# Kernel optimization log

Hardware: AMD Instinct MI355X
Metric: run time of the kernel (lower is better)

Reference implementation:

```python
import jax, jax.numpy as jnp
import numpy as np

ALPHA = 1.0
BLOCK = 128  # row block size for the pairwise L1 reduction


def _pairwise_score(features, a):
    # score[i, j] = sum_k |f[i,k] - f[j,k]| * a[k]
    # computed in row blocks to avoid the O(n^2*d) broadcast intermediate
    n, d = features.shape
    av = a[:, 0]  # [d]
    fb = features.reshape(n // BLOCK, BLOCK, d)

    def blk(fblk):  # fblk: [B, d]
        diff = jnp.abs(fblk[:, None, :] - features[None, :, :])  # [B, n, d]
        return jnp.einsum('bnd,d->bn', diff, av)                  # [B, n]

    return jax.lax.map(blk, fb).reshape(n, n)


def setup_inputs() -> dict:
    key = jax.random.key(0)
    n, d = 8192, 256
    features = jax.random.normal(key, (n, d), dtype=jnp.float32)
    a = jnp.full((d, 1), 0.01, dtype=jnp.float32)  # nn.init.constant_(a, 0.01)
    return {"features": features, "a": a}


def reference(features, a):
    score = _pairwise_score(features, a)                 # [n, n]
    adjacency = jnp.exp(-ALPHA * jax.nn.relu(score))     # [n, n]
    # D^{-1/2} A D^{-1/2} via row/col elementwise scaling (== diag mm mm)
    dsq = jnp.sum(adjacency, axis=1) ** -0.5             # [n]
    normalized = dsq[:, None] * adjacency * dsq[None, :]
    return (normalized, adjacency)
```

## Files before the change

kernel.cpp:

```cpp
#include <hip/hip_runtime.h>
#include <math.h>

typedef unsigned int uint;
typedef float f32x4 __attribute__((ext_vector_type(4)));

__device__ __forceinline__ uint fenc(float f) {
    uint u = __float_as_uint(f);
    return (u & 0x80000000u) ? ~u : (u | 0x80000000u);
}
__device__ __forceinline__ float fdec(uint u) {
    uint v = (u & 0x80000000u) ? (u & 0x7FFFFFFFu) : ~u;
    return __uint_as_float(v);
}

__device__ __forceinline__ void ntst(float* p, float a, float b, float c, float d) {
    f32x4 t; t.x = a; t.y = b; t.z = c; t.w = d;
    __builtin_nontemporal_store(t, (f32x4*)p);
}

__global__ __launch_bounds__(256) void init_kernel(uint* __restrict__ flags,
                                                   const float* __restrict__ A,
                                                   int d)
{
    const int t = threadIdx.x;
    if (t == 0) { flags[0] = 0u; flags[1] = 0xFFFFFFFFu; flags[2] = 0u; }
    __syncthreads();
    for (int k = t; k < d; k += 256)
        if (A[k] < 0.f) atomicOr(&flags[0], 1u);
}

__global__ __launch_bounds__(256) void minmax_kernel(const float* __restrict__ F,
                                                     const float* __restrict__ A,
                                                     uint* __restrict__ flags,
                                                     int n, int d)
{
    const int total4 = n * d / 4;
    float lmin = 3.4e38f, lmax = -3.4e38f;
    for (int e4 = blockIdx.x * 256 + threadIdx.x; e4 < total4; e4 += gridDim.x * 256) {
        int e = e4 * 4;
        int dk = e % d;
        float4 f = *(const float4*)(F + e);
        float4 a = *(const float4*)(A + dk);
        float g0 = fabsf(a.x) * f.x, g1 = fabsf(a.y) * f.y;
        float g2 = fabsf(a.z) * f.z, g3 = fabsf(a.w) * f.w;
        lmin = fminf(lmin, fminf(fminf(g0, g1), fminf(g2, g3)));
        lmax = fmaxf(lmax, fmaxf(fmaxf(g0, g1), fmaxf(g2, g3)));
    }
    #pragma unroll
    for (int m = 1; m < 64; m <<= 1) {
        lmin = fminf(lmin, __shfl_xor(lmin, m));
        lmax = fmaxf(lmax, __shfl_xor(lmax, m));
    }
    if ((threadIdx.x & 63) == 0) {
        atomicMin(&flags[1], fenc(lmin));
        atomicMax(&flags[2], fenc(lmax));
    }
}

__global__ __launch_bounds__(256) void quant_kernel(const float* __restrict__ F,
                                                    const float* __restrict__ A,
                                                    const uint* __restrict__ flags,
                                                    uint* __restrict__ Q,
                                                    float* __restrict__ rowsum,
                                                    int n, int d)
{
    const int t = threadIdx.x;
    const int r = blockIdx.x * 32 + (t & 31);
    if (t < 32) rowsum[blockIdx.x * 32 + t] = 0.f;
    const int kqb = t >> 5;
    const int d4 = d >> 2;
    const float gmin = fdec(flags[1]), gmax = fdec(flags[2]);
    const float span = gmax - gmin;
    const float inv = span > 0.f ? 255.f / span : 0.f;
    for (int kq = kqb; kq < d4; kq += 8) {
        float4 f = *(const float4*)(F + (size_t)r * d + kq * 4);
        float4 a = *(const float4*)(A + kq * 4);
        uint q0 = 0, q1 = 0, q2 = 0, q3 = 0;
        if (a.x > 0.f) q0 = (uint)fminf(fmaxf((a.x * f.x - gmin) * inv + 0.5f, 0.f), 255.f);
        if (a.y > 0.f) q1 = (uint)fminf(fmaxf((a.y * f.y - gmin) * inv + 0.5f, 0.f), 255.f);
        if (a.z > 0.f) q2 = (uint)fminf(fmaxf((a.z * f.z - gmin) * inv + 0.5f, 0.f), 255.f);
        if (a.w > 0.f) q3 = (uint)fminf(fmaxf((a.w * f.w - gmin) * inv + 0.5f, 0.f), 255.f);
        Q[(size_t)kq * n + r] = q0 | (q1 << 8) | (q2 << 16) | (q3 << 24);
    }
}

__device__ __forceinline__ void sad_core(const uint* __restrict__ Q, int n, int chunks,
                                         int i0, int j0, int t,
                                         uint (&acc)[8][8],
                                         uint (&As)[16][128], uint (&Bs)[16][128])
{
    const int tx = t & 15, ty = t >> 4;
    const int kk0 = t >> 5;
    const int col = 4 * (t & 31);

    uint4 sa[2], sb[2];
    #pragma unroll
    for (int j = 0; j < 2; ++j) {
        size_t g = ((size_t)(kk0 + 8 * j)) * n;
        sa[j] = *(const uint4*)(Q + g + i0 + col);
        sb[j] = *(const uint4*)(Q + g + j0 + col);
    }

    for (int c = 0; c < chunks; ++c) {
        ((uint4*)&As[0][0])[t]       = sa[0];
        ((uint4*)&As[0][0])[256 + t] = sa[1];
        ((uint4*)&Bs[0][0])[t]       = sb[0];
        ((uint4*)&Bs[0][0])[256 + t] = sb[1];
        __syncthreads();

        if (c + 1 < chunks) {
            #pragma unroll
            for (int j = 0; j < 2; ++j) {
                size_t g = ((size_t)((c + 1) * 16 + kk0 + 8 * j)) * n;
                sa[j] = *(const uint4*)(Q + g + i0 + col);
                sb[j] = *(const uint4*)(Q + g + j0 + col);
            }
        }

        #pragma unroll
        for (int kk = 0; kk < 16; ++kk) {
            uint ar[8], br[8];
            *(uint4*)&ar[0] = *(const uint4*)&As[kk][4 * ty];
            *(uint4*)&ar[4] = *(const uint4*)&As[kk][64 + 4 * ty];
            *(uint4*)&br[0] = *(const uint4*)&Bs[kk][4 * tx];
            *(uint4*)&br[4] = *(const uint4*)&Bs[kk][64 + 4 * tx];
            #pragma unroll
            for (int m = 0; m < 8; ++m)
                #pragma unroll
                for (int cc = 0; cc < 8; ++cc)
                    acc[m][cc] = __builtin_amdgcn_sad_u8(ar[m], br[cc], acc[m][cc]);
        }
        __syncthreads();
    }
}

__device__ __forceinline__ void tri_decode(int b, int& bx, int& by) {
    bx = (int)((sqrtf(8.f * (float)b + 1.f) - 1.f) * 0.5f);
    while ((bx + 1) * (bx + 2) / 2 <= b) ++bx;
    while (bx * (bx + 1) / 2 > b) --bx;
    by = b - bx * (bx + 1) / 2;
}

__global__ __launch_bounds__(256, 3) void pass1_sad(const uint* __restrict__ Q,
                                                    const uint* __restrict__ flags,
                                                    float* __restrict__ adj,
                                                    float* __restrict__ rowsum,
                                                    int n, int d)
{
    if (flags[0] != 0u) return;

    __shared__ uint As[16][128];
    __shared__ uint Bs[16][128];

    int bx, by; tri_decode(blockIdx.x, bx, by);
    const int t = threadIdx.x, tx = t & 15, ty = t >> 4;
    const int i0 = by * 128, j0 = bx * 128;
    const bool diag = (bx == by);

    const float gmin = fdec(flags[1]), gmax = fdec(flags[2]);
    const float nstep = (gmin - gmax) * (1.f / 255.f);

    uint acc[8][8] = {};
    sad_core(Q, n, (d >> 2) >> 4, i0, j0, t, acc, As, Bs);

    #pragma unroll
    for (int m = 0; m < 8; ++m)
        #pragma unroll
        for (int cc = 0; cc < 8; ++cc)
            acc[m][cc] = __float_as_uint(__expf(nstep * (float)acc[m][cc]));

    #pragma unroll
    for (int m = 0; m < 8; ++m) {
        const int row = i0 + (m >> 2) * 64 + 4 * ty + (m & 3);
        #pragma unroll
        for (int qh = 0; qh < 2; ++qh)
            ntst(adj + (size_t)row * n + j0 + qh * 64 + 4 * tx,
                 __uint_as_float(acc[m][qh * 4 + 0]),
                 __uint_as_float(acc[m][qh * 4 + 1]),
                 __uint_as_float(acc[m][qh * 4 + 2]),
                 __uint_as_float(acc[m][qh * 4 + 3]));
    }

    if (!diag) {
        #pragma unroll
        for (int h = 0; h < 2; ++h)
            #pragma unroll
            for (int qh = 0; qh < 2; ++qh)
                #pragma unroll
                for (int cc = 0; cc < 4; ++cc) {
                    const int r = j0 + qh * 64 + 4 * tx + cc;
                    ntst(adj + (size_t)r * n + i0 + 64 * h + 4 * ty,
                         __uint_as_float(acc[4 * h + 0][qh * 4 + cc]),
                         __uint_as_float(acc[4 * h + 1][qh * 4 + cc]),
                         __uint_as_float(acc[4 * h + 2][qh * 4 + cc]),
                         __uint_as_float(acc[4 * h + 3][qh * 4 + cc]));
                }
    }

    #pragma unroll
    for (int m = 0; m < 8; ++m) {
        const int row = i0 + (m >> 2) * 64 + 4 * ty + (m & 3);
        float rs = 0.f;
        #pragma unroll
        for (int cc = 0; cc < 8; ++cc) rs += __uint_as_float(acc[m][cc]);
        rs += __shfl_xor(rs, 1);
        rs += __shfl_xor(rs, 2);
        rs += __shfl_xor(rs, 4);
        rs += __shfl_xor(rs, 8);
        if (tx == 0) atomicAdd(rowsum + row, rs);
    }

    if (!diag) {
        float cs[8];
        #pragma unroll
        for (int cc = 0; cc < 8; ++cc) {
            float s = 0.f;
            #pragma unroll
            for (int m = 0; m < 8; ++m) s += __uint_as_float(acc[m][cc]);
            s += __shfl_xor(s, 16);
            s += __shfl_xor(s, 32);
            cs[cc] = s;
        }
        if ((t & 48) == 0) {
            #pragma unroll
            for (int qh = 0; qh < 2; ++qh)
                #pragma unroll
                for (int cc = 0; cc < 4; ++cc)
                    atomicAdd(rowsum + j0 + qh * 64 + 4 * tx + cc, cs[qh * 4 + cc]);
        }
    }
}

__global__ __launch_bounds__(256) void adj_fp32_kernel(
    const float* __restrict__ F, const float* __restrict__ A,
    const uint* __restrict__ flags,
    float* __restrict__ adj, float* __restrict__ rowsum, int n, int d)
{
    if (flags[0] == 0u) return;

    __shared__ __align__(16) float As[32][132];
    __shared__ __align__(16) float Bs[32][132];
    __shared__ float aw[256];

    const int t  = threadIdx.x;
    const int tx = t & 15;
    const int ty = t >> 4;
    const int nb = n / 128;

    for (int k = t; k < d; k += 256) aw[k] = A[k];

    for (int bt = blockIdx.x; bt < nb * nb; bt += gridDim.x) {
        const int i0 = (bt / nb) * 128;
        const int j0 = (bt % nb) * 128;

        float acc[2][2][4][4] = {};
        const int lr = t >> 3;
        const int lk = (t & 7) << 2;

        for (int kc = 0; kc < d; kc += 32) {
            __syncthreads();
            #pragma unroll
            for (int s = 0; s < 4; ++s) {
                int r = lr + 32 * s;
                float4 v = *(const float4*)(F + (size_t)(i0 + r) * d + kc + lk);
                As[lk + 0][r] = v.x; As[lk + 1][r] = v.y;
                As[lk + 2][r] = v.z; As[lk + 3][r] = v.w;
                float4 u = *(const float4*)(F + (size_t)(j0 + r) * d + kc + lk);
                Bs[lk + 0][r] = u.x; Bs[lk + 1][r] = u.y;
                Bs[lk + 2][r] = u.z; Bs[lk + 3][r] = u.w;
            }
            __syncthreads();

            #pragma unroll
            for (int k = 0; k < 32; ++k) {
                float av[2][4], bv[2][4];
                *(float4*)&av[0][0] = *(const float4*)&As[k][4 * ty];
                *(float4*)&av[1][0] = *(const float4*)&As[k][64 + 4 * ty];
                *(float4*)&bv[0][0] = *(const float4*)&Bs[k][4 * tx];
                *(float4*)&bv[1][0] = *(const float4*)&Bs[k][64 + 4 * tx];
                const float w = aw[kc + k];
                #pragma unroll
                for (int p = 0; p < 2; ++p)
                    #pragma unroll
                    for (int m = 0; m < 4; ++m)
                        #pragma unroll
                        for (int q = 0; q < 2; ++q)
                            #pragma unroll
                            for (int c = 0; c < 4; ++c)
                                acc[p][q][m][c] += fabsf(av[p][m] - bv[q][c]) * w;
            }
        }

        #pragma unroll
        for (int p = 0; p < 2; ++p) {
            #pragma unroll
            for (int m = 0; m < 4; ++m) {
                const int row = i0 + p * 64 + ty * 4 + m;
                float rs = 0.f;
                #pragma unroll
                for (int q = 0; q < 2; ++q) {
                    float4 v;
                    v.x = __expf(-fmaxf(acc[p][q][m][0], 0.f));
                    v.y = __expf(-fmaxf(acc[p][q][m][1], 0.f));
                    v.z = __expf(-fmaxf(acc[p][q][m][2], 0.f));
                    v.w = __expf(-fmaxf(acc[p][q][m][3], 0.f));
                    rs += (v.x + v.y) + (v.z + v.w);
                    *(float4*)(adj + (size_t)row * n + j0 + q * 64 + tx * 4) = v;
                }
                rs += __shfl_xor(rs, 1);
                rs += __shfl_xor(rs, 2);
                rs += __shfl_xor(rs, 4);
                rs += __shfl_xor(rs, 8);
                if (tx == 0) atomicAdd(rowsum + row, rs);
            }
        }
        __syncthreads();
    }
}

__global__ __launch_bounds__(256) void dsq_kernel(
    const float* __restrict__ rowsum, float* __restrict__ dsq, int n)
{
    int i = blockIdx.x * 256 + threadIdx.x;
    if (i < n) dsq[i] = 1.f / sqrtf(rowsum[i]);
}

__global__ __launch_bounds__(256) void norm_kernel(
    const float* __restrict__ adj, const float* __restrict__ dsq,
    float* __restrict__ out, int n)
{
    const int i = blockIdx.y;
    const float di = dsq[i];
    const int j0 = blockIdx.x * 4096 + threadIdx.x * 4;
    #pragma unroll
    for (int k = 0; k < 4; ++k) {
        const int j = j0 + k * 1024;
        if (j >= n) return;
        f32x4 a = __builtin_nontemporal_load((const f32x4*)(adj + (size_t)i * n + j));
        float4 dj = *(const float4*)(dsq + j);
        ntst(out + (size_t)i * n + j,
             di * a.x * dj.x, di * a.y * dj.y, di * a.z * dj.z, di * a.w * dj.w);
    }
}

extern "C" void kernel_launch(void* const* d_in, const int* in_sizes, int n_in,
                              void* d_out, int out_size, void* d_ws, size_t ws_size,
                              hipStream_t stream)
{
    const float* F = (const float*)d_in[0];
    const float* A = (const float*)d_in[1];
    const int d = in_sizes[1];
    const int n = in_sizes[0] / d;

    float* nrm    = (float*)d_out;
    float* adj    = nrm + (size_t)n * n;
    uint*  flags  = (uint*)d_ws;
    float* rowsum = (float*)d_ws + 8;
    float* dsq    = rowsum + n;
    uint* Q = (uint*)d_out;

    init_kernel<<<dim3(1), dim3(256), 0, stream>>>(flags, A, d);
    minmax_kernel<<<dim3(256), dim3(256), 0, stream>>>(F, A, flags, n, d);
    quant_kernel<<<dim3(n / 32), dim3(256), 0, stream>>>(F, A, flags, Q, rowsum, n, d);

    const int nb = n / 128;
    const int tri = nb * (nb + 1) / 2;
    pass1_sad<<<dim3(tri), dim3(256), 0, stream>>>(Q, flags, adj, rowsum, n, d);
    adj_fp32_kernel<<<dim3(1024), dim3(256), 0, stream>>>(F, A, flags, adj, rowsum, n, d);

    dsq_kernel<<<dim3((n + 255) / 256), dim3(256), 0, stream>>>(rowsum, dsq, n);

    dim3 gridN((n + 4095) / 4096, n);
    norm_kernel<<<gridN, dim3(256), 0, stream>>>(adj, dsq, nrm, n);
}
```

Baseline: 299.5 us.

## Double-buffer SAD tiles, stage transposed stores via LDS, fuse dsq into norm

The SAD main loop now uses double-buffered shared memory, so the next chunk is written while the current one is consumed, with one barrier per chunk instead of two. The mirrored (transposed) adjacency writes for off-diagonal tiles are staged through a padded LDS buffer so that each row's global stores are contiguous rather than strided. The dsq kernel is removed and norm_kernel computes rsqrt of the row sums inline. The adj_fp32 grid is cut from 1024 to 304 blocks. Doubling shared memory may lower occupancy, and rsqrt is recomputed for every element.

```diff
diff --git a/kernel.cpp b/kernel.cpp
--- a/kernel.cpp
+++ b/kernel.cpp
@@ -84,56 +84,6 @@
     }
 }
 
-__device__ __forceinline__ void sad_core(const uint* __restrict__ Q, int n, int chunks,
-                                         int i0, int j0, int t,
-                                         uint (&acc)[8][8],
-                                         uint (&As)[16][128], uint (&Bs)[16][128])
-{
-    const int tx = t & 15, ty = t >> 4;
-    const int kk0 = t >> 5;
-    const int col = 4 * (t & 31);
-
-    uint4 sa[2], sb[2];
-    #pragma unroll
-    for (int j = 0; j < 2; ++j) {
-        size_t g = ((size_t)(kk0 + 8 * j)) * n;
-        sa[j] = *(const uint4*)(Q + g + i0 + col);
-        sb[j] = *(const uint4*)(Q + g + j0 + col);
-    }
-
-    for (int c = 0; c < chunks; ++c) {
-        ((uint4*)&As[0][0])[t]       = sa[0];
-        ((uint4*)&As[0][0])[256 + t] = sa[1];
-        ((uint4*)&Bs[0][0])[t]       = sb[0];
-        ((uint4*)&Bs[0][0])[256 + t] = sb[1];
-        __syncthreads();
-
-        if (c + 1 < chunks) {
-            #pragma unroll
-            for (int j = 0; j < 2; ++j) {
-                size_t g = ((size_t)((c + 1) * 16 + kk0 + 8 * j)) * n;
-                sa[j] = *(const uint4*)(Q + g + i0 + col);
-                sb[j] = *(const uint4*)(Q + g + j0 + col);
-            }
-        }
-
-        #pragma unroll
-        for (int kk = 0; kk < 16; ++kk) {
-            uint ar[8], br[8];
-            *(uint4*)&ar[0] = *(const uint4*)&As[kk][4 * ty];
-            *(uint4*)&ar[4] = *(const uint4*)&As[kk][64 + 4 * ty];
-            *(uint4*)&br[0] = *(const uint4*)&Bs[kk][4 * tx];
-            *(uint4*)&br[4] = *(const uint4*)&Bs[kk][64 + 4 * tx];
-            #pragma unroll
-            for (int m = 0; m < 8; ++m)
-                #pragma unroll
-                for (int cc = 0; cc < 8; ++cc)
-                    acc[m][cc] = __builtin_amdgcn_sad_u8(ar[m], br[cc], acc[m][cc]);
-        }
-        __syncthreads();
-    }
-}
-
 __device__ __forceinline__ void tri_decode(int b, int& bx, int& by) {
     bx = (int)((sqrtf(8.f * (float)b + 1.f) - 1.f) * 0.5f);
     while ((bx + 1) * (bx + 2) / 2 <= b) ++bx;
@@ -149,19 +99,65 @@
 {
     if (flags[0] != 0u) return;
 
-    __shared__ uint As[16][128];
-    __shared__ uint Bs[16][128];
+    __shared__ uint S[2][2][16][128];
 
     int bx, by; tri_decode(blockIdx.x, bx, by);
     const int t = threadIdx.x, tx = t & 15, ty = t >> 4;
     const int i0 = by * 128, j0 = bx * 128;
     const bool diag = (bx == by);
+    const int chunks = (d >> 2) >> 4;
 
     const float gmin = fdec(flags[1]), gmax = fdec(flags[2]);
     const float nstep = (gmin - gmax) * (1.f / 255.f);
 
     uint acc[8][8] = {};
-    sad_core(Q, n, (d >> 2) >> 4, i0, j0, t, acc, As, Bs);
+
+    const int kk0 = t >> 5;
+    const int col = 4 * (t & 31);
+
+    uint4 sa[2], sb[2];
+    #pragma unroll
+    for (int j = 0; j < 2; ++j) {
+        size_t g = ((size_t)(kk0 + 8 * j)) * n;
+        sa[j] = *(const uint4*)(Q + g + i0 + col);
+        sb[j] = *(const uint4*)(Q + g + j0 + col);
+    }
+    ((uint4*)&S[0][0][0][0])[t]       = sa[0];
+    ((uint4*)&S[0][0][0][0])[256 + t] = sa[1];
+    ((uint4*)&S[0][1][0][0])[t]       = sb[0];
+    ((uint4*)&S[0][1][0][0])[256 + t] = sb[1];
+    __syncthreads();
+
+    for (int c = 0; c < chunks; ++c) {
+        const int cur = c & 1;
+        if (c + 1 < chunks) {
+            #pragma unroll
+            for (int j = 0; j < 2; ++j) {
+                size_t g = ((size_t)((c + 1) * 16 + kk0 + 8 * j)) * n;
+                sa[j] = *(const uint4*)(Q + g + i0 + col);
+                sb[j] = *(const uint4*)(Q + g + j0 + col);
+            }
+            ((uint4*)&S[cur ^ 1][0][0][0])[t]       = sa[0];
+            ((uint4*)&S[cur ^ 1][0][0][0])[256 + t] = sa[1];
+            ((uint4*)&S[cur ^ 1][1][0][0])[t]       = sb[0];
+            ((uint4*)&S[cur ^ 1][1][0][0])[256 + t] = sb[1];
+        }
+
+        #pragma unroll
+        for (int kk = 0; kk < 16; ++kk) {
+            uint ar[8], br[8];
+            *(uint4*)&ar[0] = *(const uint4*)&S[cur][0][kk][4 * ty];
+            *(uint4*)&ar[4] = *(const uint4*)&S[cur][0][kk][64 + 4 * ty];
+            *(uint4*)&br[0] = *(const uint4*)&S[cur][1][kk][4 * tx];
+            *(uint4*)&br[4] = *(const uint4*)&S[cur][1][kk][64 + 4 * tx];
+            #pragma unroll
+            for (int m = 0; m < 8; ++m)
+                #pragma unroll
+                for (int cc = 0; cc < 8; ++cc)
+                    acc[m][cc] = __builtin_amdgcn_sad_u8(ar[m], br[cc], acc[m][cc]);
+        }
+        __syncthreads();
+    }
 
     #pragma unroll
     for (int m = 0; m < 8; ++m)
@@ -182,19 +178,32 @@
     }
 
     if (!diag) {
-        #pragma unroll
-        for (int h = 0; h < 2; ++h)
-            #pragma unroll
-            for (int qh = 0; qh < 2; ++qh)
-                #pragma unroll
-                for (int cc = 0; cc < 4; ++cc) {
-                    const int r = j0 + qh * 64 + 4 * tx + cc;
-                    ntst(adj + (size_t)r * n + i0 + 64 * h + 4 * ty,
-                         __uint_as_float(acc[4 * h + 0][qh * 4 + cc]),
-                         __uint_as_float(acc[4 * h + 1][qh * 4 + cc]),
-                         __uint_as_float(acc[4 * h + 2][qh * 4 + cc]),
-                         __uint_as_float(acc[4 * h + 3][qh * 4 + cc]));
+        float* T = (float*)&S[0][0][0][0];
+        const int TP = 130;
+        #pragma unroll
+        for (int s = 0; s < 4; ++s) {
+            __syncthreads();
+            const int qh = s >> 1;
+            if ((tx >> 3) == (s & 1)) {
+                #pragma unroll
+                for (int m = 0; m < 8; ++m) {
+                    const int drow = (m >> 2) * 64 + 4 * ty + (m & 3);
+                    #pragma unroll
+                    for (int cc = 0; cc < 4; ++cc) {
+                        const int c = 4 * (tx & 7) + cc;
+                        T[c * TP + drow] = __uint_as_float(acc[m][qh * 4 + cc]);
+                    }
                 }
+            }
+            __syncthreads();
+            const int c = t >> 3, rg = (t & 7) * 16;
+            float* dst = adj + (size_t)(j0 + 32 * s + c) * n + i0 + rg;
+            const float* src = T + c * TP + rg;
+            #pragma unroll
+            for (int v = 0; v < 4; ++v)
+                ntst(dst + 4 * v, src[4 * v + 0], src[4 * v + 1],
+                                  src[4 * v + 2], src[4 * v + 3]);
+        }
     }
 
     #pragma unroll
@@ -318,28 +327,22 @@
     }
 }
 
-__global__ __launch_bounds__(256) void dsq_kernel(
-    const float* __restrict__ rowsum, float* __restrict__ dsq, int n)
-{
-    int i = blockIdx.x * 256 + threadIdx.x;
-    if (i < n) dsq[i] = 1.f / sqrtf(rowsum[i]);
-}
-
 __global__ __launch_bounds__(256) void norm_kernel(
-    const float* __restrict__ adj, const float* __restrict__ dsq,
+    const float* __restrict__ adj, const float* __restrict__ rowsum,
     float* __restrict__ out, int n)
 {
     const int i = blockIdx.y;
-    const float di = dsq[i];
+    const float di = rsqrtf(rowsum[i]);
     const int j0 = blockIdx.x * 4096 + threadIdx.x * 4;
     #pragma unroll
     for (int k = 0; k < 4; ++k) {
         const int j = j0 + k * 1024;
         if (j >= n) return;
         f32x4 a = __builtin_nontemporal_load((const f32x4*)(adj + (size_t)i * n + j));
-        float4 dj = *(const float4*)(dsq + j);
+        float4 rj = *(const float4*)(rowsum + j);
         ntst(out + (size_t)i * n + j,
-             di * a.x * dj.x, di * a.y * dj.y, di * a.z * dj.z, di * a.w * dj.w);
+             di * a.x * rsqrtf(rj.x), di * a.y * rsqrtf(rj.y),
+             di * a.z * rsqrtf(rj.z), di * a.w * rsqrtf(rj.w));
     }
 }
 
@@ -356,7 +359,6 @@
     float* adj    = nrm + (size_t)n * n;
     uint*  flags  = (uint*)d_ws;
     float* rowsum = (float*)d_ws + 8;
-    float* dsq    = rowsum + n;
     uint* Q = (uint*)d_out;
 
     init_kernel<<<dim3(1), dim3(256), 0, stream>>>(flags, A, d);
@@ -366,10 +368,8 @@
     const int nb = n / 128;
     const int tri = nb * (nb + 1) / 2;
     pass1_sad<<<dim3(tri), dim3(256), 0, stream>>>(Q, flags, adj, rowsum, n, d);
-    adj_fp32_kernel<<<dim3(1024), dim3(256), 0, stream>>>(F, A, flags, adj, rowsum, n, d);
-
-    dsq_kernel<<<dim3((n + 255) / 256), dim3(256), 0, stream>>>(rowsum, dsq, n);
+    adj_fp32_kernel<<<dim3(304), dim3(256), 0, stream>>>(F, A, flags, adj, rowsum, n, d);
 
     dim3 gridN((n + 4095) / 4096, n);
-    norm_kernel<<<gridN, dim3(256), 0, stream>>>(adj, dsq, nrm, n);
-}
+    norm_kernel<<<gridN, dim3(256), 0, stream>>>(adj, rowsum, nrm, n);
+}
```

Result: slower. 396.4 us (+32.3%).
